# Performance work log

Measured on AMD Instinct MI355X. Metric: run time of the kernel, lower is better.

The kernel has to match this reference:

```python
import jax, jax.numpy as jnp
import numpy as np

T, B, C, L = 2000, 64, 256, 200  # frames, batch, vocab, target length
NEG_INF = jnp.float32(-1e30)


def setup_inputs() -> dict:
    key = jax.random.key(0)
    k1, k2 = jax.random.split(key)
    inputs = jax.random.normal(k1, (T, B, C), dtype=jnp.float32)
    targets = jax.random.randint(k2, (B, L), 0, C, dtype=jnp.int64)
    return {"inputs": inputs, "targets": targets}


def _transducer_loss(inputs, targets):
    # log-normalize emissions, then batch-major: [B, T, C]
    log_probs = jax.nn.log_softmax(inputs, axis=2)
    log_probs = jnp.transpose(log_probs, (1, 0, 2))
    Bn, Tn, Cn = log_probs.shape
    Ln = targets.shape[1]
    # emission score of target token l at frame t: emit[b, t, l]
    idx = jnp.broadcast_to(targets[:, None, :], (Bn, Tn, Ln))
    emit = jnp.take_along_axis(log_probs, idx, axis=2)  # [B, T, L]

    # Monotonic-alignment forward DP (gtn forward_score over the
    # composed emissions/alignment graph): at each frame either stay on the
    # current target token or advance to the next one; every token emitted >=1 frame.
    # alpha[b, l] = logsumexp over alignments of frames 0..t ending at token l.
    alpha0 = jnp.full((Bn, Ln), NEG_INF, dtype=log_probs.dtype).at[:, 0].set(emit[:, 0, 0])

    def step(alpha, e_t):
        shifted = jnp.concatenate(
            [jnp.full((Bn, 1), NEG_INF, dtype=alpha.dtype), alpha[:, :-1]], axis=1
        )
        alpha = e_t + jnp.logaddexp(alpha, shifted)
        return alpha, None

    emit_t_major = jnp.swapaxes(emit, 0, 1)  # [T, B, L]
    alpha, _ = jax.lax.scan(step, alpha0, emit_t_major[1:])

    # negative log-likelihood (scale = -1), averaged over the batch
    return jnp.mean(-alpha[:, -1])


def reference(inputs, targets):
    return _transducer_loss(inputs, targets)
```

## Files before the change

kernel.cpp:

```cpp
#include <hip/hip_runtime.h>

#define T_FRAMES 2000
#define BATCH    64
#define CVOC     256
#define LTGT     200
#define EPAD     200
#define SEG      20
#define NSEGH    50
#define NEG_INF  (-1e30f)
#define INV_LN2  1.4426950408889634f
#define LN2      0.6931471805599453f

#if __has_builtin(__builtin_amdgcn_exp2f)
__device__ __forceinline__ float fexp2(float x) { return __builtin_amdgcn_exp2f(x); }
#else
__device__ __forceinline__ float fexp2(float x) { return exp2f(x); }
#endif
#if __has_builtin(__builtin_amdgcn_logf)
__device__ __forceinline__ float flog2(float x) { return __builtin_amdgcn_logf(x); }
#else
__device__ __forceinline__ float flog2(float x) { return log2f(x); }
#endif

typedef unsigned long long u64;

struct __align__(8) H4 { _Float16 x, y, z, w; };
union HU { u64 u; H4 h; };

__device__ __forceinline__ void stage_seg(u64* dst, const char* gseg, int lane) {
#if __has_builtin(__builtin_amdgcn_global_load_lds)
#pragma unroll
    for (int k = 0; k < 8; ++k)
        __builtin_amdgcn_global_load_lds(
            (const __attribute__((address_space(1))) void*)(gseg + k * 1024 + lane * 16),
            (__attribute__((address_space(3))) void*)((char*)dst + k * 1024),
            16, 0, 0);
#else
#pragma unroll
    for (int k = 0; k < 8; ++k) {
        const u64* gq = (const u64*)(gseg + k * 1024);
        u64* lq = dst + k * 128;
        lq[lane * 2]     = gq[lane * 2];
        lq[lane * 2 + 1] = gq[lane * 2 + 1];
    }
#endif
}

__device__ __forceinline__ float dpp_shr1_zero(float v) {
    return __int_as_float(__builtin_amdgcn_update_dpp(
        0, __float_as_int(v), 0x138, 0xF, 0xF, true));
}
__device__ __forceinline__ int dpp_shr1_zero_i(int v) {
    return __builtin_amdgcn_update_dpp(0, v, 0x138, 0xF, 0xF, true);
}
__device__ __forceinline__ float dpp_shl1_zero(float v) {
    return __int_as_float(__builtin_amdgcn_update_dpp(
        0, __float_as_int(v), 0x130, 0xF, 0xF, true));
}
__device__ __forceinline__ int dpp_shl1_zero_i(int v) {
    return __builtin_amdgcn_update_dpp(0, v, 0x130, 0xF, 0xF, true);
}
template <int CTRL, int RMASK>
__device__ __forceinline__ float dpp_term(float v) {
    return __int_as_float(__builtin_amdgcn_update_dpp(
        0, __float_as_int(v), CTRL, RMASK, 0xF, true));
}
__device__ __forceinline__ float wave_max(float v) {
    v = fmaxf(v, dpp_term<0x111, 0xF>(v));
    v = fmaxf(v, dpp_term<0x112, 0xF>(v));
    v = fmaxf(v, dpp_term<0x114, 0xF>(v));
    v = fmaxf(v, dpp_term<0x118, 0xF>(v));
    v = fmaxf(v, dpp_term<0x142, 0xA>(v));
    v = fmaxf(v, dpp_term<0x143, 0xC>(v));
    return __int_as_float(__builtin_amdgcn_readlane(__float_as_int(v), 63));
}
__device__ __forceinline__ float wave_sum(float v) {
    v += dpp_term<0x111, 0xF>(v);
    v += dpp_term<0x112, 0xF>(v);
    v += dpp_term<0x114, 0xF>(v);
    v += dpp_term<0x118, 0xF>(v);
    v += dpp_term<0x142, 0xA>(v);
    v += dpp_term<0x143, 0xC>(v);
    return __int_as_float(__builtin_amdgcn_readlane(__float_as_int(v), 63));
}

__global__ __launch_bounds__(256) void emit_kernel(const float* __restrict__ x,
                                                   const int* __restrict__ targets,
                                                   _Float16* __restrict__ emit) {
    __shared__ float s[16][CVOC];
    const int w = threadIdx.x >> 6;
    const int lane = threadIdx.x & 63;
    const int r0 = blockIdx.x * 16 + w * 4;
    const int li = (lane < 50) ? lane : 49;

    float4 v[4];
#pragma unroll
    for (int k = 0; k < 4; ++k)
        v[k] = ((const float4*)(x + (size_t)(r0 + k) * CVOC))[lane];
    int4 tg[4];
#pragma unroll
    for (int k = 0; k < 4; ++k)
        tg[k] = ((const int4*)(targets + ((r0 + k) & 63) * LTGT))[li];

    float lse2[4];
#pragma unroll
    for (int k = 0; k < 4; ++k) {
        v[k].x *= INV_LN2; v[k].y *= INV_LN2; v[k].z *= INV_LN2; v[k].w *= INV_LN2;
        float m = fmaxf(fmaxf(v[k].x, v[k].y), fmaxf(v[k].z, v[k].w));
        m = wave_max(m);
        float ss = fexp2(v[k].x - m) + fexp2(v[k].y - m) +
                   fexp2(v[k].z - m) + fexp2(v[k].w - m);
        ss = wave_sum(ss);
        lse2[k] = m + flog2(ss);
        ((float4*)&s[w * 4 + k][lane * 4])[0] = v[k];
    }

#pragma unroll
    for (int k = 0; k < 4; ++k) {
        if (lane < 50) {
            const int r = r0 + k;
            const int t = r >> 6;
            const int b = r & 63;
            H4 h;
            h.x = (_Float16)fexp2(s[w * 4 + k][tg[k].x] - lse2[k]);
            h.y = (_Float16)fexp2(s[w * 4 + k][tg[k].y] - lse2[k]);
            h.z = (_Float16)fexp2(s[w * 4 + k][tg[k].z] - lse2[k]);
            h.w = (_Float16)fexp2(s[w * 4 + k][tg[k].w] - lse2[k]);
            ((H4*)(emit + ((size_t)b * T_FRAMES + t) * EPAD))[lane] = h;
        }
    }
}

__device__ __forceinline__ void renormF(float& z0, float& z1, float& z2, float& z3,
                                        int& A) {
    const float m4 = fmaxf(fmaxf(z0, z1), fmaxf(z2, z3));
    const int Ap = dpp_shr1_zero_i(A);
    const bool act = (m4 > 0.0f);
    const int sh = act ? (127 - ((__float_as_int(m4) >> 23) & 255)) : 0;
    z0 = ldexpf(z0, sh); z1 = ldexpf(z1, sh);
    z2 = ldexpf(z2, sh); z3 = ldexpf(z3, sh);
    A = act ? (A - sh) : Ap;
}
__device__ __forceinline__ void renormB(float& z0, float& z1, float& z2, float& z3,
                                        int& A) {
    const float m4 = fmaxf(fmaxf(z0, z1), fmaxf(z2, z3));
    const int Ap = dpp_shl1_zero_i(A);
    const bool act = (m4 > 0.0f);
    const int sh = act ? (127 - ((__float_as_int(m4) >> 23) & 255)) : 0;
    z0 = ldexpf(z0, sh); z1 = ldexpf(z1, sh);
    z2 = ldexpf(z2, sh); z3 = ldexpf(z3, sh);
    A = act ? (A - sh) : Ap;
}

__global__ __launch_bounds__(128, 1) void dp2_kernel(const _Float16* __restrict__ emit,
                                                     float4* __restrict__ fz,
                                                     int* __restrict__ fA,
                                                     float4* __restrict__ bz,
                                                     int* __restrict__ bA) {
    __shared__ u64 buf[2][1024];
    const int bid = blockIdx.x;
    const bool bwd = bid >= BATCH;
    const int b = bwd ? (bid - BATCH) : bid;
    const int wv = threadIdx.x >> 6;
    const int lane = threadIdx.x & 63;
    const _Float16* base = emit + (size_t)b * T_FRAMES * EPAD;
    const char* bbase = (const char*)base;
    const int fi = (lane < 50) ? lane : 49;


    float z0 = 0.0f, z1 = 0.0f, z2 = 0.0f, z3 = 0.0f;
    int A = 0, dA = 0;
    float r0 = 0.0f, r1 = 0.0f, r2 = 0.0f, r3 = 0.0f;
    int rA = 0;

    if (wv == 0) {
        if (!bwd) {
            const float e00 = (float)base[0];
            z0 = (lane == 0) ? e00 : 0.0f;
            renormF(z0, z1, z2, z3, A);
            dA = dpp_shr1_zero_i(A) - A;
        } else {
            z3 = (lane == 49) ? 1.0f : 0.0f;
        }
    } else {
        const size_t sb0 = (size_t)(bwd ? 1980 : 1) * 400;
        stage_seg(buf[0], bbase + sb0, lane);
    }
    __syncthreads();

#define DPF_STEP(eu, cap, j)                                          \
    {                                                                 \
        HU _hu; _hu.u = (eu);                                         \
        const float pv = dpp_shr1_zero(z3);                           \
        const float pe = ldexpf(pv, dA);                              \
        const float e0 = (float)_hu.h.x;                              \
        const float e1 = (float)_hu.h.y;                              \
        const float e2 = (float)_hu.h.z;                              \
        const float e3 = (float)_hu.h.w;                              \
        const float n0 = e0 * (z0 + pe);                              \
        const float n1 = e1 * (z1 + z0);                              \
        const float n2 = e2 * (z2 + z1);                              \
        const float n3 = e3 * (z3 + z2);                              \
        z0 = n0; z1 = n1; z2 = n2; z3 = n3;                           \
        if ((cap) && (j) == 18) { r0 = z0; r1 = z1; r2 = z2; r3 = z3; rA = A; } \
        if (((j) & 3) == 3) { renormF(z0, z1, z2, z3, A);             \
                              dA = dpp_shr1_zero_i(A) - A; }          \
    }
#define DPB_STEP(eu, j)                                               \
    {                                                                 \
        HU _hu; _hu.u = (eu);                                         \
        const float e0 = (float)_hu.h.x;                              \
        const float e1 = (float)_hu.h.y;                              \
        const float e2 = (float)_hu.h.z;                              \
        const float e3 = (float)_hu.h.w;                              \
        const float w0 = z0 * e0;                                     \
        const float w1 = z1 * e1;                                     \
        const float w2 = z2 * e2;                                     \
        const float w3 = z3 * e3;                                     \
        const float q  = dpp_shl1_zero(w0);                           \
        const float pe = ldexpf(q, dA);                               \
        z0 = w0 + w1; z1 = w1 + w2; z2 = w2 + w3; z3 = w3 + pe;       \
        if (((j) & 3) == 3) { renormB(z0, z1, z2, z3, A);             \
                              dA = dpp_shl1_zero_i(A) - A; }          \
    }

    for (int s = 0; s < NSEGH; ++s) {
        const u64* cur = buf[s & 1];
        if (wv == 1) {
            if (s + 1 < NSEGH) {
                const size_t sb =
                    (size_t)(bwd ? (1980 - 20 * (s + 1)) : (1 + 20 * (s + 1))) * 400;
                stage_seg(buf[(s + 1) & 1], bbase + sb, lane);
            }
        } else if (!bwd) {
            const bool cap = (s == NSEGH - 1);
#pragma unroll
            for (int j = 0; j < SEG; ++j) DPF_STEP(cur[j * 50 + fi], cap, j);
        } else {
#pragma unroll
            for (int j = 0; j < SEG; ++j) DPB_STEP(cur[(19 - j) * 50 + fi], j);
        }
        __syncthreads();
    }
#undef DPF_STEP
#undef DPB_STEP

    if (wv == 0) {
        if (!bwd) {
            fz[b * 64 + lane] = make_float4(r0, r1, r2, r3);
            fA[b * 64 + lane] = rA;
        } else {
            bz[b * 64 + lane] = make_float4(z0, z1, z2, z3);
            bA[b * 64 + lane] = A;
        }
    }
}

__global__ __launch_bounds__(64) void combine_kernel(const float4* __restrict__ fz,
                                                     const int* __restrict__ fA,
                                                     const float4* __restrict__ bz,
                                                     const int* __restrict__ bA,
                                                     float* __restrict__ part) {
    const int b = blockIdx.x;
    const int lane = threadIdx.x;
    const float4 f = fz[b * 64 + lane];
    const float4 g = bz[b * 64 + lane];
    const float s = f.x * g.x + f.y * g.y + f.z * g.z + f.w * g.w;
    float tl = (lane < 50 && s > 0.0f)
                   ? flog2(s) + (float)(fA[b * 64 + lane] + bA[b * 64 + lane])
                   : -3.0e38f;
    float m = tl;
#pragma unroll
    for (int d = 1; d < 64; d <<= 1) m = fmaxf(m, __shfl_xor(m, d, 64));
    float p = fexp2(tl - m);
#pragma unroll
    for (int d = 1; d < 64; d <<= 1) p += __shfl_xor(p, d, 64);
    if (lane == 0) part[b] = -(m + flog2(p)) * LN2;
}

__global__ __launch_bounds__(64) void reduce_kernel(const float* __restrict__ part,
                                                    float* __restrict__ out) {
    float v = part[threadIdx.x];
#pragma unroll
    for (int s = 1; s < 64; s <<= 1) v += __shfl_xor(v, s, 64);
    if (threadIdx.x == 0) out[0] = v * (1.0f / BATCH);
}

__device__ __forceinline__ float lae(float a, float b) {
    float m = fmaxf(a, b);
    float d = fminf(a, b) - m;
    return m + __logf(1.0f + __expf(d));
}

__global__ __launch_bounds__(256) void lse_kernel(const float* __restrict__ x,
                                                  float* __restrict__ lse) {
    const int wave = threadIdx.x >> 6;
    const int lane = threadIdx.x & 63;
    const int r = blockIdx.x * 4 + wave;
    float4 v = ((const float4*)(x + (size_t)r * CVOC))[lane];
    float m = fmaxf(fmaxf(v.x, v.y), fmaxf(v.z, v.w));
#pragma unroll
    for (int s = 1; s < 64; s <<= 1) m = fmaxf(m, __shfl_xor(m, s, 64));
    float ssum = __expf(v.x - m) + __expf(v.y - m) + __expf(v.z - m) + __expf(v.w - m);
#pragma unroll
    for (int s = 1; s < 64; s <<= 1) ssum += __shfl_xor(ssum, s, 64);
    if (lane == 0) {
        const int t = r >> 6;
        const int b = r & 63;
        lse[b * T_FRAMES + t] = m + __logf(ssum);
    }
}

__global__ __launch_bounds__(64) void dp_slow_kernel(const float* __restrict__ x,
                                                     const int* __restrict__ targets,
                                                     const float* __restrict__ lse,
                                                     float* __restrict__ part) {
    __shared__ float s_lse[T_FRAMES];
    const int b = blockIdx.x;
    const int lane = threadIdx.x;
    for (int i = lane; i < T_FRAMES; i += 64) s_lse[i] = lse[b * T_FRAMES + i];
    const int* tg = targets + b * LTGT;
    const int l0 = lane * 4;
    const int i0 = tg[(l0 + 0 < LTGT) ? (l0 + 0) : (LTGT - 1)];
    const int i1 = tg[(l0 + 1 < LTGT) ? (l0 + 1) : (LTGT - 1)];
    const int i2 = tg[(l0 + 2 < LTGT) ? (l0 + 2) : (LTGT - 1)];
    const int i3 = tg[(l0 + 3 < LTGT) ? (l0 + 3) : (LTGT - 1)];
    const float* xb = x + b * CVOC;
    __syncthreads();
    float a0 = (lane == 0) ? (xb[i0] - s_lse[0]) : NEG_INF;
    float a1 = NEG_INF, a2 = NEG_INF, a3 = NEG_INF;
    const float* rA = xb + (size_t)1 * BATCH * CVOC;
    float pa0 = rA[i0], pa1 = rA[i1], pa2 = rA[i2], pa3 = rA[i3];
    const float* rB = xb + (size_t)2 * BATCH * CVOC;
    float pb0 = rB[i0], pb1 = rB[i1], pb2 = rB[i2], pb3 = rB[i3];
#define DP_STEP(e0, e1, e2, e3, tt)                                   \
    {                                                                 \
        const float ls = s_lse[tt];                                   \
        float prev = __shfl_up(a3, 1, 64);                            \
        if (lane == 0) prev = NEG_INF;                                \
        const float n0 = ((e0) - ls) + lae(a0, prev);                 \
        const float n1 = ((e1) - ls) + lae(a1, a0);                   \
        const float n2 = ((e2) - ls) + lae(a2, a1);                   \
        const float n3 = ((e3) - ls) + lae(a3, a2);                   \
        a0 = n0; a1 = n1; a2 = n2; a3 = n3;                           \
    }
    int t = 1;
    while (t < T_FRAMES) {
        DP_STEP(pa0, pa1, pa2, pa3, t);
        {
            const int tn = (t + 2 < T_FRAMES) ? (t + 2) : (T_FRAMES - 1);
            const float* r = xb + (size_t)tn * BATCH * CVOC;
            pa0 = r[i0]; pa1 = r[i1]; pa2 = r[i2]; pa3 = r[i3];
        }
        ++t;
        if (t >= T_FRAMES) break;
        DP_STEP(pb0, pb1, pb2, pb3, t);
        {
            const int tn = (t + 2 < T_FRAMES) ? (t + 2) : (T_FRAMES - 1);
            const float* r = xb + (size_t)tn * BATCH * CVOC;
            pb0 = r[i0]; pb1 = r[i1]; pb2 = r[i2]; pb3 = r[i3];
        }
        ++t;
    }
#undef DP_STEP
    const float resv = __shfl(a3, 49, 64);
    if (lane == 0) part[b] = -resv;
}

extern "C" void kernel_launch(void* const* d_in, const int* in_sizes, int n_in,
                              void* d_out, int out_size, void* d_ws, size_t ws_size,
                              hipStream_t stream) {
    const float* x = (const float*)d_in[0];
    const int* targets = (const int*)d_in[1];
    float* out = (float*)d_out;

    const size_t emit_bytes = (size_t)BATCH * T_FRAMES * EPAD * sizeof(_Float16);
    const size_t off_part = emit_bytes + 4096;
    const size_t off_fz   = emit_bytes + 8192;
    const size_t off_fA   = off_fz + (size_t)BATCH * 64 * 16;
    const size_t off_bz   = off_fA + (size_t)BATCH * 64 * 4;
    const size_t off_bA   = off_bz + (size_t)BATCH * 64 * 16;
    const size_t need     = off_bA + (size_t)BATCH * 64 * 4 + 4096;

    if (ws_size >= need) {
        _Float16* emit = (_Float16*)d_ws;
        float*  part = (float*)((char*)d_ws + off_part);
        float4* fz   = (float4*)((char*)d_ws + off_fz);
        int*    fAi  = (int*)((char*)d_ws + off_fA);
        float4* bz   = (float4*)((char*)d_ws + off_bz);
        int*    bAi  = (int*)((char*)d_ws + off_bA);
        emit_kernel<<<T_FRAMES * BATCH / 16, 256, 0, stream>>>(x, targets, emit);
        dp2_kernel<<<2 * BATCH, 128, 0, stream>>>(emit, fz, fAi, bz, bAi);
        combine_kernel<<<BATCH, 64, 0, stream>>>(fz, fAi, bz, bAi, part);
        reduce_kernel<<<1, 64, 0, stream>>>(part, out);
    } else {
        float* lse = (float*)d_ws;
        float* part = lse + (size_t)BATCH * T_FRAMES;
        lse_kernel<<<T_FRAMES * BATCH / 4, 256, 0, stream>>>(x, lse);
        dp_slow_kernel<<<BATCH, 64, 0, stream>>>(x, targets, lse, part);
        reduce_kernel<<<1, 64, 0, stream>>>(part, out);
    }
}
```

Measured before the change: 238.3 us.

## Interleave forward and backward DP chains in one wavefront per batch item

Merges the separate forward and backward DP blocks into a single block per batch element. One wave runs both recurrences interleaved step by step, while the other wave stages both emission segments into a doubled shared buffer. The two independent dependency chains are meant to hide each other's ALU and DPP latency, and the launch needs half as many blocks. In exchange the kernel uses more registers and twice the LDS, and each segment does twice the serial work inside one wave.

```diff
diff --git a/kernel.cpp b/kernel.cpp
--- a/kernel.cpp
+++ b/kernel.cpp
@@ -157,54 +157,50 @@
                                                      int* __restrict__ fA,
                                                      float4* __restrict__ bz,
                                                      int* __restrict__ bA) {
-    __shared__ u64 buf[2][1024];
-    const int bid = blockIdx.x;
-    const bool bwd = bid >= BATCH;
-    const int b = bwd ? (bid - BATCH) : bid;
+    __shared__ u64 buf[2][2][1024];
+    const int b = blockIdx.x;
     const int wv = threadIdx.x >> 6;
     const int lane = threadIdx.x & 63;
     const _Float16* base = emit + (size_t)b * T_FRAMES * EPAD;
     const char* bbase = (const char*)base;
     const int fi = (lane < 50) ? lane : 49;
 
-
-    float z0 = 0.0f, z1 = 0.0f, z2 = 0.0f, z3 = 0.0f;
-    int A = 0, dA = 0;
+    float f0 = 0.0f, f1 = 0.0f, f2 = 0.0f, f3 = 0.0f;
+    int Af = 0, dAf = 0;
     float r0 = 0.0f, r1 = 0.0f, r2 = 0.0f, r3 = 0.0f;
     int rA = 0;
+    float g0 = 0.0f, g1 = 0.0f, g2 = 0.0f, g3 = 0.0f;
+    int Ab = 0, dAb = 0;
 
     if (wv == 0) {
-        if (!bwd) {
-            const float e00 = (float)base[0];
-            z0 = (lane == 0) ? e00 : 0.0f;
-            renormF(z0, z1, z2, z3, A);
-            dA = dpp_shr1_zero_i(A) - A;
-        } else {
-            z3 = (lane == 49) ? 1.0f : 0.0f;
-        }
+        const float e00 = (float)base[0];
+        f0 = (lane == 0) ? e00 : 0.0f;
+        renormF(f0, f1, f2, f3, Af);
+        dAf = dpp_shr1_zero_i(Af) - Af;
+        g3 = (lane == 49) ? 1.0f : 0.0f;
     } else {
-        const size_t sb0 = (size_t)(bwd ? 1980 : 1) * 400;
-        stage_seg(buf[0], bbase + sb0, lane);
+        stage_seg(buf[0][0], bbase + (size_t)1 * 400, lane);
+        stage_seg(buf[0][1], bbase + (size_t)1980 * 400, lane);
     }
     __syncthreads();
 
 #define DPF_STEP(eu, cap, j)                                          \
     {                                                                 \
         HU _hu; _hu.u = (eu);                                         \
-        const float pv = dpp_shr1_zero(z3);                           \
-        const float pe = ldexpf(pv, dA);                              \
+        const float pv = dpp_shr1_zero(f3);                           \
+        const float pe = ldexpf(pv, dAf);                             \
         const float e0 = (float)_hu.h.x;                              \
         const float e1 = (float)_hu.h.y;                              \
         const float e2 = (float)_hu.h.z;                              \
         const float e3 = (float)_hu.h.w;                              \
-        const float n0 = e0 * (z0 + pe);                              \
-        const float n1 = e1 * (z1 + z0);                              \
-        const float n2 = e2 * (z2 + z1);                              \
-        const float n3 = e3 * (z3 + z2);                              \
-        z0 = n0; z1 = n1; z2 = n2; z3 = n3;                           \
-        if ((cap) && (j) == 18) { r0 = z0; r1 = z1; r2 = z2; r3 = z3; rA = A; } \
-        if (((j) & 3) == 3) { renormF(z0, z1, z2, z3, A);             \
-                              dA = dpp_shr1_zero_i(A) - A; }          \
+        const float n0 = e0 * (f0 + pe);                              \
+        const float n1 = e1 * (f1 + f0);                              \
+        const float n2 = e2 * (f2 + f1);                              \
+        const float n3 = e3 * (f3 + f2);                              \
+        f0 = n0; f1 = n1; f2 = n2; f3 = n3;                           \
+        if ((cap) && (j) == 18) { r0 = f0; r1 = f1; r2 = f2; r3 = f3; rA = Af; } \
+        if (((j) & 3) == 3) { renormF(f0, f1, f2, f3, Af);            \
+                              dAf = dpp_shr1_zero_i(Af) - Af; }       \
     }
 #define DPB_STEP(eu, j)                                               \
     {                                                                 \
@@ -213,32 +209,41 @@
         const float e1 = (float)_hu.h.y;                              \
         const float e2 = (float)_hu.h.z;                              \
         const float e3 = (float)_hu.h.w;                              \
-        const float w0 = z0 * e0;                                     \
-        const float w1 = z1 * e1;                                     \
-        const float w2 = z2 * e2;                                     \
-        const float w3 = z3 * e3;                                     \
+        const float w0 = g0 * e0;                                     \
+        const float w1 = g1 * e1;                                     \
+        const float w2 = g2 * e2;                                     \
+        const float w3 = g3 * e3;                                     \
         const float q  = dpp_shl1_zero(w0);                           \
-        const float pe = ldexpf(q, dA);                               \
-        z0 = w0 + w1; z1 = w1 + w2; z2 = w2 + w3; z3 = w3 + pe;       \
-        if (((j) & 3) == 3) { renormB(z0, z1, z2, z3, A);             \
-                              dA = dpp_shl1_zero_i(A) - A; }          \
+        const float pe = ldexpf(q, dAb);                              \
+        g0 = w0 + w1; g1 = w1 + w2; g2 = w2 + w3; g3 = w3 + pe;       \
+        if (((j) & 3) == 3) { renormB(g0, g1, g2, g3, Ab);            \
+                              dAb = dpp_shl1_zero_i(Ab) - Ab; }       \
     }
 
     for (int s = 0; s < NSEGH; ++s) {
-        const u64* cur = buf[s & 1];
+        const u64* cf = buf[s & 1][0];
+        const u64* cb = buf[s & 1][1];
         if (wv == 1) {
             if (s + 1 < NSEGH) {
-                const size_t sb =
-                    (size_t)(bwd ? (1980 - 20 * (s + 1)) : (1 + 20 * (s + 1))) * 400;
-                stage_seg(buf[(s + 1) & 1], bbase + sb, lane);
+                stage_seg(buf[(s + 1) & 1][0],
+                          bbase + (size_t)(1 + 20 * (s + 1)) * 400, lane);
+                stage_seg(buf[(s + 1) & 1][1],
+                          bbase + (size_t)(1980 - 20 * (s + 1)) * 400, lane);
             }
-        } else if (!bwd) {
+        } else {
+            u64 ef[SEG], eb[SEG];
+#pragma unroll
+            for (int j = 0; j < SEG; ++j) {
+                ef[j] = cf[j * 50 + fi];
+                eb[j] = cb[(19 - j) * 50 + fi];
+            }
+            __builtin_amdgcn_sched_barrier(0);
             const bool cap = (s == NSEGH - 1);
 #pragma unroll
-            for (int j = 0; j < SEG; ++j) DPF_STEP(cur[j * 50 + fi], cap, j);
-        } else {
-#pragma unroll
-            for (int j = 0; j < SEG; ++j) DPB_STEP(cur[(19 - j) * 50 + fi], j);
+            for (int j = 0; j < SEG; ++j) {
+                DPF_STEP(ef[j], cap, j);
+                DPB_STEP(eb[j], j);
+            }
         }
         __syncthreads();
     }
@@ -246,13 +251,10 @@
 #undef DPB_STEP
 
     if (wv == 0) {
-        if (!bwd) {
-            fz[b * 64 + lane] = make_float4(r0, r1, r2, r3);
-            fA[b * 64 + lane] = rA;
-        } else {
-            bz[b * 64 + lane] = make_float4(z0, z1, z2, z3);
-            bA[b * 64 + lane] = A;
-        }
+        fz[b * 64 + lane] = make_float4(r0, r1, r2, r3);
+        fA[b * 64 + lane] = rA;
+        bz[b * 64 + lane] = make_float4(g0, g1, g2, g3);
+        bA[b * 64 + lane] = Ab;
     }
 }
 
@@ -390,7 +392,7 @@
         float4* bz   = (float4*)((char*)d_ws + off_bz);
         int*    bAi  = (int*)((char*)d_ws + off_bA);
         emit_kernel<<<T_FRAMES * BATCH / 16, 256, 0, stream>>>(x, targets, emit);
-        dp2_kernel<<<2 * BATCH, 128, 0, stream>>>(emit, fz, fAi, bz, bAi);
+        dp2_kernel<<<BATCH, 128, 0, stream>>>(emit, fz, fAi, bz, bAi);
         combine_kernel<<<BATCH, 64, 0, stream>>>(fz, fAi, bz, bAi, part);
         reduce_kernel<<<1, 64, 0, stream>>>(part, out);
     } else {
```

Measured after the change: 264.3 us. 10.9% more time.
